# Kernel tuning notes

Measured on AMD Instinct MI355X. Metric: run time of the kernel, lower is better.

## Reference

```python
import jax, jax.numpy as jnp
import numpy as np

LEFT = 16  # attention window size (previous `left` symbols incl. current)


def _make_history(symbols, left):
    """contexts[b, t, j] = symbols[b, t - (left-1-j)] for j in [0,left),
    padded with symbols[b, 0] for out-of-range positions (pad = symbols[:, :1])."""
    B, T = symbols.shape
    # (T, left) gather index matrix
    idx = jnp.arange(T)[:, None] - (left - 1 - jnp.arange(left))[None, :]
    valid = idx >= 0
    idx_c = jnp.clip(idx, 0, T - 1)
    ctx = symbols[:, idx_c]                                   # (B, T, left)
    pad = symbols[:, :1][:, :, None]                          # (B, 1, 1)
    return jnp.where(valid[None, :, :], ctx, pad)             # (B, T, left)


def setup_inputs() -> dict:
    key = jax.random.key(0)
    k1, k2, k3, k4 = jax.random.split(key, 4)
    B, T, V, D = 8, 2048, 256, 512
    symbols = jax.random.randint(k1, (B, T), 0, V, dtype=jnp.int32)
    encodings = jax.random.normal(k2, (B, T, D), dtype=jnp.float32)
    # keras 'uniform' initializer: U(-0.05, 0.05)
    M = jax.random.uniform(k3, (V, D), minval=-0.05, maxval=0.05, dtype=jnp.float32)
    C = jax.random.uniform(k4, (V, D), minval=-0.05, maxval=0.05, dtype=jnp.float32)
    return {"symbols": symbols, "encodings": encodings, "M": M, "C": C}


def reference(symbols, encodings, M, C):
    contexts = _make_history(symbols, LEFT)                   # (B, T, L) int
    Mg = M[contexts]                                          # (B, T, L, D)
    Cg = C[contexts]                                          # (B, T, L, D)
    scores = jnp.einsum('btld,btd->btl', Mg, encodings)       # (B, T, L)
    p = jax.nn.softmax(scores, axis=-1)                       # (B, T, L)
    compressed = jnp.einsum('btl,btld->btd', p, Cg)           # (B, T, D)
    output = jnp.concatenate([compressed, encodings], axis=-1)  # (B, T, 2D)
    return output, p
```

## Files before the change

### kernel.cpp

```cpp
#include <hip/hip_runtime.h>
#include <hip/hip_bf16.h>

#define B_ 8
#define T_ 2048
#define V_ 256
#define D_ 512
#define LEFT_ 16

typedef float f32x4 __attribute__((ext_vector_type(4)));
typedef short bf16x8 __attribute__((ext_vector_type(8)));
typedef unsigned long long u64;
union FragU { unsigned u[4]; u64 ull[2]; bf16x8 v; };

__device__ __forceinline__ unsigned pack_bf2(float a, float b) {
    __hip_bfloat162 h = __float22bfloat162_rn(make_float2(a, b));
    union { __hip_bfloat162 h; unsigned u; } c; c.h = h; return c.u;
}

__global__ __launch_bounds__(512)
void attn_cell_kernel(const int* __restrict__ symbols,
                      const float* __restrict__ encodings,
                      const float* __restrict__ M,
                      const float* __restrict__ C,
                      float* __restrict__ out,
                      float* __restrict__ p_out) {
    __shared__ __align__(16) float sp[8 * 16 * 36];

    const int tid  = threadIdx.x;
    const int lane = tid & 63;
    const int w    = tid >> 6;
    const int q    = lane >> 4;
    const int t    = lane & 15;

    const int blk = blockIdx.x;
    const int b   = blk >> 7;
    const int t0  = (blk & 127) * 16;
    const int* symrow = symbols + b * T_;
    const size_t rowbase = (size_t)b * T_ + t0;

    int sa[2];
    #pragma unroll
    for (int g = 0; g < 2; ++g) {
        int pos = t0 + t + 16 * g - (LEFT_ - 1);
        pos = max(pos, 0); pos = min(pos, T_ - 1);
        sa[g] = symrow[pos];
    }
    int sb[8];
    #pragma unroll
    for (int e = 0; e < 8; ++e) {
        const int j = 4 * q + (e & 3) + 16 * (e >> 2);
        int pos = t0 + j - (LEFT_ - 1);
        pos = max(pos, 0); pos = min(pos, T_ - 1);
        sb[e] = symrow[pos];
    }

    FragU bf[2];
    {
        const float* ebase = encodings + (rowbase + t) * D_;
        float* obase = out + (rowbase + t) * 1024 + D_;
        #pragma unroll
        for (int kc = 0; kc < 2; ++kc) {
            const int d0 = 64 * w + 32 * kc + 4 * q;
            const float4 e0 = *(const float4*)(ebase + d0);
            const float4 e1 = *(const float4*)(ebase + d0 + 16);
            *(float4*)(obase + d0)      = e0;
            *(float4*)(obase + d0 + 16) = e1;
            bf[kc].u[0] = pack_bf2(e0.x, e0.y); bf[kc].u[1] = pack_bf2(e0.z, e0.w);
            bf[kc].u[2] = pack_bf2(e1.x, e1.y); bf[kc].u[3] = pack_bf2(e1.z, e1.w);
        }
    }

    FragU afc[4];
    #pragma unroll
    for (int m = 0; m < 4; ++m) {
        const int dA = (w * 4 + m) * 16 + t;
        float c[8];
        #pragma unroll
        for (int e = 0; e < 8; ++e)
            c[e] = C[(size_t)sb[e] * D_ + dA];
        afc[m].u[0] = pack_bf2(c[0], c[1]); afc[m].u[1] = pack_bf2(c[2], c[3]);
        afc[m].u[2] = pack_bf2(c[4], c[5]); afc[m].u[3] = pack_bf2(c[6], c[7]);
    }

    f32x4 acc0 = {0.f, 0.f, 0.f, 0.f}, acc1 = {0.f, 0.f, 0.f, 0.f};
    #pragma unroll
    for (int kc = 0; kc < 2; ++kc) {
        const int k0 = 64 * w + 32 * kc + 4 * q;
        {
            const float* ma = M + (size_t)sa[0] * D_ + k0;
            const float4 x0 = *(const float4*)ma;
            const float4 x1 = *(const float4*)(ma + 16);
            FragU af;
            af.u[0] = pack_bf2(x0.x, x0.y); af.u[1] = pack_bf2(x0.z, x0.w);
            af.u[2] = pack_bf2(x1.x, x1.y); af.u[3] = pack_bf2(x1.z, x1.w);
            acc0 = __builtin_amdgcn_mfma_f32_16x16x32_bf16(af.v, bf[kc].v, acc0, 0, 0, 0);
        }
        {
            const float* ma = M + (size_t)sa[1] * D_ + k0;
            const float4 x0 = *(const float4*)ma;
            const float4 x1 = *(const float4*)(ma + 16);
            FragU af;
            af.u[0] = pack_bf2(x0.x, x0.y); af.u[1] = pack_bf2(x0.z, x0.w);
            af.u[2] = pack_bf2(x1.x, x1.y); af.u[3] = pack_bf2(x1.z, x1.w);
            acc1 = __builtin_amdgcn_mfma_f32_16x16x32_bf16(af.v, bf[kc].v, acc1, 0, 0, 0);
        }
    }
    *(f32x4*)&sp[(w * 16 + t) * 36 + 4 * q]      = acc0;
    *(f32x4*)&sp[(w * 16 + t) * 36 + 16 + 4 * q] = acc1;

    __syncthreads();

    FragU pf;
    {
        f32x4 s0 = *(const f32x4*)&sp[t * 36 + 4 * q];
        f32x4 s1 = *(const f32x4*)&sp[t * 36 + 16 + 4 * q];
        #pragma unroll
        for (int w2 = 1; w2 < 8; ++w2) {
            s0 += *(const f32x4*)&sp[(w2 * 16 + t) * 36 + 4 * q];
            s1 += *(const f32x4*)&sp[(w2 * 16 + t) * 36 + 16 + 4 * q];
        }
        float mx = -3.0e38f;
        #pragma unroll
        for (int r = 0; r < 4; ++r) {
            if ((unsigned)(4 * q + r - t) < 16u)      mx = fmaxf(mx, s0[r]);
            if ((unsigned)(4 * q + r + 16 - t) < 16u) mx = fmaxf(mx, s1[r]);
        }
        mx = fmaxf(mx, __shfl_xor(mx, 16));
        mx = fmaxf(mx, __shfl_xor(mx, 32));
        float p0[4], p1[4];
        float sum = 0.f;
        #pragma unroll
        for (int r = 0; r < 4; ++r) {
            const bool m0 = (unsigned)(4 * q + r - t) < 16u;
            const bool m1 = (unsigned)(4 * q + r + 16 - t) < 16u;
            p0[r] = m0 ? __expf(s0[r] - mx) : 0.f;
            p1[r] = m1 ? __expf(s1[r] - mx) : 0.f;
            sum += p0[r] + p1[r];
        }
        sum += __shfl_xor(sum, 16);
        sum += __shfl_xor(sum, 32);
        const float inv = 1.f / sum;
        #pragma unroll
        for (int r = 0; r < 4; ++r) { p0[r] *= inv; p1[r] *= inv; }

        if (w == 0) {
            #pragma unroll
            for (int r = 0; r < 4; ++r) {
                const int j0 = 4 * q + r;
                if ((unsigned)(j0 - t) < 16u)
                    p_out[(rowbase + t) * 16 + (j0 - t)] = p0[r];
                else
                    p_out[(rowbase + t) * 16 + (j0 + 16 - t)] = p1[r];
            }
        }
        pf.u[0] = pack_bf2(p0[0], p0[1]); pf.u[1] = pack_bf2(p0[2], p0[3]);
        pf.u[2] = pack_bf2(p1[0], p1[1]); pf.u[3] = pack_bf2(p1[2], p1[3]);
    }

    #pragma unroll
    for (int m = 0; m < 4; ++m) {
        f32x4 o = {0.f, 0.f, 0.f, 0.f};
        o = __builtin_amdgcn_mfma_f32_16x16x32_bf16(afc[m].v, pf.v, o, 0, 0, 0);
        float* ob = out + (rowbase + t) * 1024 + (w * 4 + m) * 16 + 4 * q;
        *(float4*)ob = make_float4(o[0], o[1], o[2], o[3]);
    }
}

extern "C" void kernel_launch(void* const* d_in, const int* in_sizes, int n_in,
                              void* d_out, int out_size, void* d_ws, size_t ws_size,
                              hipStream_t stream) {
    const int*   symbols   = (const int*)d_in[0];
    const float* encodings = (const float*)d_in[1];
    const float* M         = (const float*)d_in[2];
    const float* C         = (const float*)d_in[3];
    float* out   = (float*)d_out;
    float* p_out = out + (size_t)B_ * T_ * 1024;

    dim3 grid(B_ * (T_ / 16));
    attn_cell_kernel<<<grid, 512, 0, stream>>>(symbols, encodings, M, C, out, p_out);
}
```

Measured before the change: 32.74 us.

## Split fused attention into score and compress kernels with FP32 sliding-window compress

```diff
diff --git a/kernel.cpp b/kernel.cpp
--- a/kernel.cpp
+++ b/kernel.cpp
@@ -9,8 +9,7 @@
 
 typedef float f32x4 __attribute__((ext_vector_type(4)));
 typedef short bf16x8 __attribute__((ext_vector_type(8)));
-typedef unsigned long long u64;
-union FragU { unsigned u[4]; u64 ull[2]; bf16x8 v; };
+union FragU { unsigned u[4]; bf16x8 v; };
 
 __device__ __forceinline__ unsigned pack_bf2(float a, float b) {
     __hip_bfloat162 h = __float22bfloat162_rn(make_float2(a, b));
@@ -18,12 +17,11 @@
 }
 
 __global__ __launch_bounds__(512)
-void attn_cell_kernel(const int* __restrict__ symbols,
-                      const float* __restrict__ encodings,
-                      const float* __restrict__ M,
-                      const float* __restrict__ C,
-                      float* __restrict__ out,
-                      float* __restrict__ p_out) {
+void score_kernel(const int* __restrict__ symbols,
+                  const float* __restrict__ encodings,
+                  const float* __restrict__ M,
+                  float* __restrict__ out,
+                  float* __restrict__ p_out) {
     __shared__ __align__(16) float sp[8 * 16 * 36];
 
     const int tid  = threadIdx.x;
@@ -44,14 +42,6 @@
         int pos = t0 + t + 16 * g - (LEFT_ - 1);
         pos = max(pos, 0); pos = min(pos, T_ - 1);
         sa[g] = symrow[pos];
-    }
-    int sb[8];
-    #pragma unroll
-    for (int e = 0; e < 8; ++e) {
-        const int j = 4 * q + (e & 3) + 16 * (e >> 2);
-        int pos = t0 + j - (LEFT_ - 1);
-        pos = max(pos, 0); pos = min(pos, T_ - 1);
-        sb[e] = symrow[pos];
     }
 
     FragU bf[2];
@@ -68,18 +58,6 @@
             bf[kc].u[0] = pack_bf2(e0.x, e0.y); bf[kc].u[1] = pack_bf2(e0.z, e0.w);
             bf[kc].u[2] = pack_bf2(e1.x, e1.y); bf[kc].u[3] = pack_bf2(e1.z, e1.w);
         }
-    }
-
-    FragU afc[4];
-    #pragma unroll
-    for (int m = 0; m < 4; ++m) {
-        const int dA = (w * 4 + m) * 16 + t;
-        float c[8];
-        #pragma unroll
-        for (int e = 0; e < 8; ++e)
-            c[e] = C[(size_t)sb[e] * D_ + dA];
-        afc[m].u[0] = pack_bf2(c[0], c[1]); afc[m].u[1] = pack_bf2(c[2], c[3]);
-        afc[m].u[2] = pack_bf2(c[4], c[5]); afc[m].u[3] = pack_bf2(c[6], c[7]);
     }
 
     f32x4 acc0 = {0.f, 0.f, 0.f, 0.f}, acc1 = {0.f, 0.f, 0.f, 0.f};
@@ -110,7 +88,6 @@
 
     __syncthreads();
 
-    FragU pf;
     {
         f32x4 s0 = *(const f32x4*)&sp[t * 36 + 4 * q];
         f32x4 s1 = *(const f32x4*)&sp[t * 36 + 16 + 4 * q];
@@ -140,29 +117,74 @@
         sum += __shfl_xor(sum, 16);
         sum += __shfl_xor(sum, 32);
         const float inv = 1.f / sum;
-        #pragma unroll
-        for (int r = 0; r < 4; ++r) { p0[r] *= inv; p1[r] *= inv; }
 
         if (w == 0) {
             #pragma unroll
             for (int r = 0; r < 4; ++r) {
                 const int j0 = 4 * q + r;
                 if ((unsigned)(j0 - t) < 16u)
-                    p_out[(rowbase + t) * 16 + (j0 - t)] = p0[r];
+                    p_out[(rowbase + t) * 16 + (j0 - t)] = p0[r] * inv;
                 else
-                    p_out[(rowbase + t) * 16 + (j0 + 16 - t)] = p1[r];
+                    p_out[(rowbase + t) * 16 + (j0 + 16 - t)] = p1[r] * inv;
             }
         }
-        pf.u[0] = pack_bf2(p0[0], p0[1]); pf.u[1] = pack_bf2(p0[2], p0[3]);
-        pf.u[2] = pack_bf2(p1[0], p1[1]); pf.u[3] = pack_bf2(p1[2], p1[3]);
-    }
-
-    #pragma unroll
-    for (int m = 0; m < 4; ++m) {
-        f32x4 o = {0.f, 0.f, 0.f, 0.f};
-        o = __builtin_amdgcn_mfma_f32_16x16x32_bf16(afc[m].v, pf.v, o, 0, 0, 0);
-        float* ob = out + (rowbase + t) * 1024 + (w * 4 + m) * 16 + 4 * q;
-        *(float4*)ob = make_float4(o[0], o[1], o[2], o[3]);
+    }
+}
+
+__global__ __launch_bounds__(256)
+void compress_kernel(const int* __restrict__ symbols,
+                     const float* __restrict__ C,
+                     const float* __restrict__ p_in,
+                     float* __restrict__ out) {
+    const int tid  = threadIdx.x;
+    const int lane = tid & 63;
+    const int w    = tid >> 6;
+
+    const int blk = blockIdx.x;
+    const int b   = blk >> 7;
+    const int tb  = (blk & 127) * 16 + w * 4;
+    const int* symrow = symbols + b * T_;
+    const size_t rowbase = (size_t)b * T_ + tb;
+    const int dof = lane * 8;
+
+    float pv[4];
+    #pragma unroll
+    for (int tk = 0; tk < 4; ++tk)
+        pv[tk] = p_in[(rowbase + tk) * 16 + (lane & 15)];
+
+    float4 a0[4], a1[4];
+    #pragma unroll
+    for (int tk = 0; tk < 4; ++tk) {
+        a0[tk] = make_float4(0.f, 0.f, 0.f, 0.f);
+        a1[tk] = make_float4(0.f, 0.f, 0.f, 0.f);
+    }
+
+    #pragma unroll
+    for (int i = 0; i < 19; ++i) {
+        int pos = tb - (LEFT_ - 1) + i;
+        pos = max(pos, 0);
+        const int sym = __builtin_amdgcn_readfirstlane(symrow[pos]);
+        const float* cr = C + (size_t)sym * D_ + dof;
+        const float4 c0 = *(const float4*)cr;
+        const float4 c1 = *(const float4*)(cr + 4);
+        #pragma unroll
+        for (int tk = 0; tk < 4; ++tk) {
+            const int sl = i - tk;
+            if (sl >= 0 && sl < 16) {
+                const float pb = __shfl(pv[tk], sl);
+                a0[tk].x += pb * c0.x; a0[tk].y += pb * c0.y;
+                a0[tk].z += pb * c0.z; a0[tk].w += pb * c0.w;
+                a1[tk].x += pb * c1.x; a1[tk].y += pb * c1.y;
+                a1[tk].z += pb * c1.z; a1[tk].w += pb * c1.w;
+            }
+        }
+    }
+
+    #pragma unroll
+    for (int tk = 0; tk < 4; ++tk) {
+        float* ob = out + (rowbase + tk) * 1024 + dof;
+        *(float4*)ob       = a0[tk];
+        *(float4*)(ob + 4) = a1[tk];
     }
 }
 
@@ -177,5 +199,6 @@
     float* p_out = out + (size_t)B_ * T_ * 1024;
 
     dim3 grid(B_ * (T_ / 16));
-    attn_cell_kernel<<<grid, 512, 0, stream>>>(symbols, encodings, M, C, out, p_out);
-}
+    score_kernel<<<grid, 512, 0, stream>>>(symbols, encodings, M, out, p_out);
+    compress_kernel<<<grid, 256, 0, stream>>>(symbols, C, p_out, out);
+}
```

Measured after the change: 39.90 us. +21.9%, slower.
